# Kernel tuning notes

Measured on AMD Instinct MI355X. Metric: run time of the kernel, lower is better.

The kernel has to match this reference:

```python
import jax, jax.numpy as jnp
import numpy as np


def setup_inputs() -> dict:
    key = jax.random.key(0)
    ks = jax.random.split(key, 9)
    B, D_IN, UNITS, TOPICS, VOCAB = 64, 512, 1024, 20, 32000
    return {
        "inputs": jax.random.normal(ks[0], (B, D_IN), jnp.float32),
        "prev_state": jax.random.normal(ks[1], (B, UNITS), jnp.float32),
        "kernel": jax.random.normal(ks[2], (D_IN, UNITS), jnp.float32) * 0.02,
        "recurrent_kernel": jax.random.normal(ks[3], (UNITS, UNITS), jnp.float32) * 0.02,
        "bernoli_kernel": jax.random.normal(ks[4], (UNITS, 1), jnp.float32) * 0.02,
        "vocab_kernel": jax.random.normal(ks[5], (UNITS, VOCAB), jnp.float32) * 0.02,
        "beta": jax.random.normal(ks[6], (TOPICS, VOCAB), jnp.float32),
        "indicators": jax.random.randint(ks[7], (B,), 0, 2, jnp.int32),
        "indices": jax.random.randint(ks[8], (B,), 0, VOCAB, jnp.int32),
    }


def reference(inputs, prev_state, kernel, recurrent_kernel, bernoli_kernel,
              vocab_kernel, beta, indicators, indices):
    # h_t = x @ W_xh + h_{t-1} @ W_hh   -> [B, units]
    next_state = inputs @ kernel + prev_state @ recurrent_kernel
    # stop-word Bernoulli prob: sigmoid(softplus(h_t @ w_b))  -> [B, 1]
    bern_p = jax.nn.sigmoid(jax.nn.softplus(next_state @ bernoli_kernel))
    bern_p = bern_p[..., None]  # [B, 1, 1]
    # deterministic sampling key (reference baseline)
    samp_key = jax.random.key(42)
    bern_samples = jax.random.bernoulli(samp_key, bern_p).astype(jnp.float32)
    # logits: [B,1,V] + (1 - l_t) * beta[T,V] -> [B, T, V]
    logits = (next_state @ vocab_kernel)[:, None, :] + (1.0 - bern_samples) * beta
    word_prob_out = jax.nn.softmax(logits, axis=-1)
    return word_prob_out, next_state
```

## Files before the change

kernel.cpp:

```cpp
#include <hip/hip_runtime.h>
#include <cstdint>
#include <cstddef>

typedef unsigned int u32;
typedef unsigned short u16;

#define NB 64
#define DIN 512
#define UNITS 1024
#define TOPICS 20
#define VOCAB 32000
#define NS_OFF ((size_t)NB * TOPICS * VOCAB)
#define ESV_PART ((size_t)NB * VOCAB)

typedef __attribute__((ext_vector_type(8))) short s16x8;
typedef __attribute__((ext_vector_type(4))) float f32x4;

__device__ __forceinline__ float bf2f(u16 h) {
    union { u32 u; float f; } c; c.u = ((u32)h) << 16; return c.f;
}
__device__ __forceinline__ u16 f2bf(float f) {
    union { float f; u32 u; } c; c.f = f;
    u32 r = c.u + 0x7FFFu + ((c.u >> 16) & 1u);
    return (u16)(r >> 16);
}
template<bool F32>
__device__ __forceinline__ float ldv(const void* p, size_t i) {
    if constexpr (F32) return ((const float*)p)[i];
    else return bf2f(((const u16*)p)[i]);
}
__device__ __forceinline__ float ldr(const void* p, size_t i, bool f32) {
    return f32 ? ((const float*)p)[i] : bf2f(((const u16*)p)[i]);
}

__device__ __forceinline__ u32 threefry_bits_partitionable(u32 i) {
    const u32 ks0 = 0u, ks1 = 42u, ks2 = 0u ^ 42u ^ 0x1BD11BDAu;
    u32 x0 = 0u + ks0, x1 = i + ks1;
#define TF_R(r) { x0 += x1; x1 = (x1 << r) | (x1 >> (32 - r)); x1 ^= x0; }
    TF_R(13) TF_R(15) TF_R(26) TF_R(6)
    x0 += ks1; x1 += ks2 + 1u;
    TF_R(17) TF_R(29) TF_R(16) TF_R(24)
    x0 += ks2; x1 += ks0 + 2u;
    TF_R(13) TF_R(15) TF_R(26) TF_R(6)
    x0 += ks0; x1 += ks1 + 3u;
    TF_R(17) TF_R(29) TF_R(16) TF_R(24)
    x0 += ks1; x1 += ks2 + 4u;
    TF_R(13) TF_R(15) TF_R(26) TF_R(6)
    x0 += ks2; x1 += ks0 + 5u;
#undef TF_R
    return x0 ^ x1;
}

__global__ __launch_bounds__(256)
void k_init(const void* __restrict__ beta, int* __restrict__ flag,
            float* __restrict__ lsum, float* __restrict__ eb) {
    int tid = threadIdx.x, lane = tid & 63, w = tid >> 6;
    __shared__ int cnt_s[4];
    int cnt = 0;
    const u32* braw = (const u32*)beta;
    for (int i = tid; i < 1024; i += 256) {
        u32 x = braw[i];
        u32 e = (x >> 7) & 0xFFu;
        cnt += (e >= 110u && e <= 132u) ? 1 : 0;
    }
    for (int off = 32; off; off >>= 1) cnt += __shfl_down(cnt, off, 64);
    if (lane == 0) cnt_s[w] = cnt;
    __syncthreads();
    int total = cnt_s[0] + cnt_s[1] + cnt_s[2] + cnt_s[3];
    bool f32 = total < 512;

    size_t base = (size_t)blockIdx.x * 2000;
    for (int i = tid; i < 2000; i += 256)
        eb[base + i] = __expf(ldr(beta, base + i, f32));

    if (blockIdx.x == 0) {
        for (int i = tid; i < NB * TOPICS; i += 256) lsum[i] = 0.f;
        if (tid == 0) flag[0] = f32 ? 1 : 0;
    }
}

template<bool F32>
__device__ void state_body(const void* xin, const void* h0, const void* Wxh,
                           const void* Whh, float* ns_p) {
    __shared__ float lx[768];
    int bid  = blockIdx.x;
    int b    = bid >> 3;
    int uq   = (bid >> 1) & 3;
    int half = bid & 1;
    int u = (uq << 8) | threadIdx.x;
    for (int i = threadIdx.x; i < 768; i += 256) {
        int kk = half * 768 + i;
        lx[i] = (kk < DIN) ? ldv<F32>(xin, (size_t)b * DIN + kk)
                           : ldv<F32>(h0,  (size_t)b * UNITS + (kk - DIN));
    }
    __syncthreads();
    float acc = 0.f;
    if (half == 0) {
#pragma unroll 8
        for (int k = 0; k < DIN; ++k) acc += lx[k] * ldv<F32>(Wxh, (size_t)k * UNITS + u);
#pragma unroll 8
        for (int k = 0; k < 256; ++k) acc += lx[DIN + k] * ldv<F32>(Whh, (size_t)k * UNITS + u);
    } else {
#pragma unroll 8
        for (int k = 0; k < 768; ++k) acc += lx[k] * ldv<F32>(Whh, (size_t)(256 + k) * UNITS + u);
    }
    ns_p[half * (NB * UNITS) + b * UNITS + u] = acc;
}
__global__ __launch_bounds__(256)
void k_state(const int* __restrict__ flag, const void* xin, const void* h0,
             const void* Wxh, const void* Whh, float* __restrict__ ns_p) {
    if (*flag) state_body<true>(xin, h0, Wxh, Whh, ns_p);
    else       state_body<false>(xin, h0, Wxh, Whh, ns_p);
}

template<bool F32>
__device__ void bern_body(const float* ns_p, const void* bk, float* coeff,
                          float* ns_f32, void* dout) {
    int b = blockIdx.x, lane = threadIdx.x;
    float s = 0.f;
#pragma unroll
    for (int i = 0; i < UNITS / 64; ++i) {
        int k = lane + (i << 6);
        int idx = b * UNITS + k;
        float v = ns_p[idx] + ns_p[NB * UNITS + idx];
        ns_f32[idx] = v;
        if constexpr (F32) ((float*)dout)[NS_OFF + idx] = v;
        else               ((u16*)dout)[NS_OFF + idx]   = f2bf(v);
        s += v * ldv<F32>(bk, k);
    }
    for (int off = 32; off; off >>= 1) s += __shfl_down(s, off, 64);
    if (lane == 0) {
        float sp = log1pf(expf(s));
        float p  = 1.f / (1.f + expf(-sp));
        u32 bits = threefry_bits_partitionable((u32)b);
        union { u32 u; float f; } c; c.u = (bits >> 9) | 0x3f800000u;
        float uni = c.f - 1.0f;
        coeff[b] = (uni < p) ? 0.f : 1.f;
    }
}
__global__ __launch_bounds__(64)
void k_bern(const int* __restrict__ flag, const float* __restrict__ ns_p,
            const void* bk, float* __restrict__ coeff,
            float* __restrict__ ns_f32, void* dout) {
    if (*flag) bern_body<true>(ns_p, bk, coeff, ns_f32, dout);
    else       bern_body<false>(ns_p, bk, coeff, ns_f32, dout);
}

#define PAD 68
#define SV_BB 4096
#define SV_SMEM_BYTES 34816

__device__ void sv_mfma_body(const short* __restrict__ ns16,
                             const short* __restrict__ Wv,
                             float* __restrict__ esv4, char* smem,
                             int pos, int kb) {
    const int tid  = threadIdx.x;
    const int lane = tid & 63;
    const int wn   = tid >> 6;
    const int g    = lane >> 4;
    const int l15  = lane & 15;

    const int v0 = pos * 64;
    const int kbase0 = kb * 256;

    const int bk_ = tid >> 3, bc_ = tid & 7;
    const short* bsrc = Wv + (size_t)(kbase0 + bk_) * VOCAB + v0
                      + ((bc_ ^ (bk_ >> 3)) << 3);
    const short* as0 = ns16 + (size_t)(l15     ) * UNITS + kbase0 + g * 8;
    const short* as1 = ns16 + (size_t)(l15 + 16) * UNITS + kbase0 + g * 8;
    const short* as2 = ns16 + (size_t)(l15 + 32) * UNITS + kbase0 + g * 8;
    const short* as3 = ns16 + (size_t)(l15 + 48) * UNITS + kbase0 + g * 8;

    float4 bE, bO;
    s16x8  aE0, aE1, aE2, aE3;
    s16x8  aO0, aO1, aO2, aO3;

    f32x4 acc[4];
#pragma unroll
    for (int m = 0; m < 4; ++m) acc[m] = (f32x4){0.f, 0.f, 0.f, 0.f};

#define LOADB(T, R)  { R = *(const float4*)(bsrc + (size_t)(T) * 32 * VOCAB); }
#define LOADA(T, A0, A1, A2, A3) {                                        \
    int ko = (T) * 32;                                                    \
    A0 = *(const s16x8*)(as0 + ko); A1 = *(const s16x8*)(as1 + ko);       \
    A2 = *(const s16x8*)(as2 + ko); A3 = *(const s16x8*)(as3 + ko); }
#define WRITEB(BUF, R)  { ((float4*)(smem + (BUF) * SV_BB))[tid] = R; }
#define COMPUTE(BUF, A0, A1, A2, A3) {                                    \
    const short* Bs = (const short*)(smem + (BUF) * SV_BB);               \
    int col = wn * 16 + l15;                                              \
    int b0  = (((col >> 3) ^ g) << 3) + (col & 7);                        \
    s16x8 bf;                                                             \
    _Pragma("unroll")                                                     \
    for (int e = 0; e < 8; ++e) bf[e] = Bs[(g * 8 + e) * 64 + b0];        \
    acc[0] = __builtin_amdgcn_mfma_f32_16x16x32_bf16(A0, bf, acc[0], 0, 0, 0); \
    acc[1] = __builtin_amdgcn_mfma_f32_16x16x32_bf16(A1, bf, acc[1], 0, 0, 0); \
    acc[2] = __builtin_amdgcn_mfma_f32_16x16x32_bf16(A2, bf, acc[2], 0, 0, 0); \
    acc[3] = __builtin_amdgcn_mfma_f32_16x16x32_bf16(A3, bf, acc[3], 0, 0, 0); }
#define VMW(N)  asm volatile("s_waitcnt vmcnt(" #N ")" ::: "memory");
#define LGK0    asm volatile("s_waitcnt lgkmcnt(0)" ::: "memory");
#define BAR     __builtin_amdgcn_s_barrier();

    LOADB(0, bE)
    LOADA(0, aE0, aE1, aE2, aE3)
    LOADB(1, bO)
    VMW(5)
    WRITEB(0, bE)
    LGK0

    LOADB(2, bE)  LOADA(1, aO0, aO1, aO2, aO3)
    BAR  VMW(5)  WRITEB(1, bO)  LGK0
    COMPUTE(0, aE0, aE1, aE2, aE3)
    LOADB(3, bO)  LOADA(2, aE0, aE1, aE2, aE3)
    BAR  VMW(5)  WRITEB(0, bE)  LGK0
    COMPUTE(1, aO0, aO1, aO2, aO3)
    LOADB(4, bE)  LOADA(3, aO0, aO1, aO2, aO3)
    BAR  VMW(5)  WRITEB(1, bO)  LGK0
    COMPUTE(2, aE0, aE1, aE2, aE3)
    LOADB(5, bO)  LOADA(4, aE0, aE1, aE2, aE3)
    BAR  VMW(5)  WRITEB(0, bE)  LGK0
    COMPUTE(3, aO0, aO1, aO2, aO3)
    LOADB(6, bE)  LOADA(5, aO0, aO1, aO2, aO3)
    BAR  VMW(5)  WRITEB(1, bO)  LGK0
    COMPUTE(4, aE0, aE1, aE2, aE3)
    LOADB(7, bO)  LOADA(6, aE0, aE1, aE2, aE3)
    BAR  VMW(5)  WRITEB(0, bE)  LGK0
    COMPUTE(5, aO0, aO1, aO2, aO3)
    LOADA(7, aO0, aO1, aO2, aO3)
    BAR  VMW(4)  WRITEB(1, bO)  LGK0
    COMPUTE(6, aE0, aE1, aE2, aE3)
    BAR  VMW(0)
    COMPUTE(7, aO0, aO1, aO2, aO3)

#undef LOADB
#undef LOADA
#undef WRITEB
#undef COMPUTE
#undef VMW
#undef LGK0
#undef BAR

    float* dst = esv4 + (size_t)kb * ESV_PART + v0;
    const int col = wn * 16 + l15;
#pragma unroll
    for (int mf = 0; mf < 4; ++mf)
#pragma unroll
        for (int r = 0; r < 4; ++r) {
            int b = mf * 16 + (lane >> 4) * 4 + r;
            dst[(size_t)b * VOCAB + col] = acc[mf][r];
        }
}

__device__ void sv_f32_body(const float* __restrict__ ns, const float* __restrict__ Wv,
                            float* __restrict__ esv4, float* As, float* Bs,
                            int pos, int kb) {
    int tid = threadIdx.x;
    int vt = tid & 7;
    int bg = tid >> 3;
    int v0 = pos * 64;
    float acc[2][8];
#pragma unroll
    for (int r = 0; r < 2; ++r)
#pragma unroll
        for (int j = 0; j < 8; ++j) acc[r][j] = 0.f;

    for (int k0 = kb * 256; k0 < kb * 256 + 256; k0 += 64) {
        __syncthreads();
        for (int e = tid; e < 1024; e += 256) {
            int row = e >> 4, c4 = e & 15;
            *(float4*)&As[row * PAD + c4 * 4] =
                *(const float4*)&ns[row * UNITS + k0 + c4 * 4];
        }
        for (int e = tid; e < 1024; e += 256) {
            int row = e >> 4, c4 = e & 15;
            *(float4*)&Bs[row * PAD + c4 * 4] =
                *(const float4*)(Wv + (size_t)(k0 + row) * VOCAB + v0 + c4 * 4);
        }
        __syncthreads();
#pragma unroll 4
        for (int u = 0; u < 64; u += 4) {
            float4 a0 = *(float4*)&As[(bg * 2 + 0) * PAD + u];
            float4 a1 = *(float4*)&As[(bg * 2 + 1) * PAD + u];
            float aa0[4] = {a0.x, a0.y, a0.z, a0.w};
            float aa1[4] = {a1.x, a1.y, a1.z, a1.w};
#pragma unroll
            for (int uu = 0; uu < 4; ++uu) {
                float4 b0 = *(float4*)&Bs[(u + uu) * PAD + vt * 8];
                float4 b1 = *(float4*)&Bs[(u + uu) * PAD + vt * 8 + 4];
                float bb[8] = {b0.x, b0.y, b0.z, b0.w, b1.x, b1.y, b1.z, b1.w};
#pragma unroll
                for (int j = 0; j < 8; ++j) {
                    acc[0][j] = fmaf(aa0[uu], bb[j], acc[0][j]);
                    acc[1][j] = fmaf(aa1[uu], bb[j], acc[1][j]);
                }
            }
        }
    }
    float* base = esv4 + (size_t)kb * ESV_PART;
#pragma unroll
    for (int r = 0; r < 2; ++r) {
        float4 e0 = {acc[r][0], acc[r][1], acc[r][2], acc[r][3]};
        float4 e1 = {acc[r][4], acc[r][5], acc[r][6], acc[r][7]};
        float* dst = base + (size_t)(bg * 2 + r) * VOCAB + v0 + vt * 8;
        *(float4*)dst = e0;
        *(float4*)(dst + 4) = e1;
    }
}

__global__ __launch_bounds__(256, 3)
void k_sv(const int* __restrict__ flag, const float* __restrict__ ns,
          const void* Wv, const void* dout, float* __restrict__ esv4, int kb) {
    __shared__ __align__(16) char smem[SV_SMEM_BYTES];
    int lin = blockIdx.x;
    int xcd = lin & 7, idx = lin >> 3;
    int pos = (xcd < 4) ? xcd * 63 + idx : 252 + (xcd - 4) * 62 + idx;
    if (*flag) {
        float* As = (float*)smem;
        sv_f32_body(ns, (const float*)Wv, esv4, As, As + 64 * PAD, pos, kb);
    } else {
        sv_mfma_body((const short*)dout + NS_OFF, (const short*)Wv, esv4, smem,
                     pos, kb);
    }
}

__global__ __launch_bounds__(256)
void k_sum(const float* __restrict__ esv4, const float* __restrict__ eb,
           const float* __restrict__ coeff, float* __restrict__ lsum) {
    int b = blockIdx.y, tid = threadIdx.x;
    float c = coeff[b];
    const float4* P0 = (const float4*)(esv4 + (size_t)b * VOCAB);
    const float4* P1 = (const float4*)(esv4 + ESV_PART + (size_t)b * VOCAB);
    const float4* P2 = (const float4*)(esv4 + 2 * ESV_PART + (size_t)b * VOCAB);
    const float4* P3 = (const float4*)(esv4 + 3 * ESV_PART + (size_t)b * VOCAB);
    int i0 = blockIdx.x * 256 + tid;
    __shared__ float red[4][TOPICS];
    int lane = tid & 63, w = tid >> 6;

    if (c != 0.f) {
        float acc[TOPICS];
#pragma unroll
        for (int t = 0; t < TOPICS; ++t) acc[t] = 0.f;
        for (int i = i0; i < VOCAB / 4; i += 4096) {
            float4 q = P0[i];
            float4 a = P1[i], d = P2[i], h = P3[i];
            q.x += a.x + d.x + h.x; q.y += a.y + d.y + h.y;
            q.z += a.z + d.z + h.z; q.w += a.w + d.w + h.w;
            float4 e;
            e.x = __expf(q.x); e.y = __expf(q.y);
            e.z = __expf(q.z); e.w = __expf(q.w);
#pragma unroll
            for (int t = 0; t < TOPICS; ++t) {
                float4 g = *(const float4*)(eb + (size_t)t * VOCAB + i * 4);
                acc[t] += e.x * g.x + e.y * g.y + e.z * g.z + e.w * g.w;
            }
        }
#pragma unroll
        for (int t = 0; t < TOPICS; ++t) {
            float v = acc[t];
            for (int off = 32; off; off >>= 1) v += __shfl_down(v, off, 64);
            if (lane == 0) red[w][t] = v;
        }
        __syncthreads();
        if (tid < TOPICS) {
            float s = red[0][tid] + red[1][tid] + red[2][tid] + red[3][tid];
            atomicAdd(&lsum[b * TOPICS + tid], s);
        }
    } else {
        float a = 0.f;
        for (int i = i0; i < VOCAB / 4; i += 4096) {
            float4 q = P0[i];
            float4 x = P1[i], d = P2[i], h = P3[i];
            q.x += x.x + d.x + h.x; q.y += x.y + d.y + h.y;
            q.z += x.z + d.z + h.z; q.w += x.w + d.w + h.w;
            a += __expf(q.x) + __expf(q.y) + __expf(q.z) + __expf(q.w);
        }
        for (int off = 32; off; off >>= 1) a += __shfl_down(a, off, 64);
        if (lane == 0) red[w][0] = a;
        __syncthreads();
        if (tid < TOPICS) {
            float s = red[0][0] + red[1][0] + red[2][0] + red[3][0];
            atomicAdd(&lsum[b * TOPICS + tid], s);
        }
    }
}

template<bool F32>
__device__ void write_body(const float* esv4, const float* eb, const float* coeff,
                           const float* lsum, void* dout) {
    int b = blockIdx.y, tid = threadIdx.x;
    int v0 = blockIdx.x * 2048 + tid * 8;
    if (v0 >= VOCAB) return;
    float c = coeff[b];
    const float* er = esv4 + (size_t)b * VOCAB + v0;
    float4 q0 = *(const float4*)er;
    float4 q1 = *(const float4*)(er + 4);
#pragma unroll
    for (int p = 1; p < 4; ++p) {
        float4 a0 = *(const float4*)(er + p * ESV_PART);
        float4 a1 = *(const float4*)(er + p * ESV_PART + 4);
        q0.x += a0.x; q0.y += a0.y; q0.z += a0.z; q0.w += a0.w;
        q1.x += a1.x; q1.y += a1.y; q1.z += a1.z; q1.w += a1.w;
    }
    float4 e0, e1;
    e0.x = __expf(q0.x); e0.y = __expf(q0.y); e0.z = __expf(q0.z); e0.w = __expf(q0.w);
    e1.x = __expf(q1.x); e1.y = __expf(q1.y); e1.z = __expf(q1.z); e1.w = __expf(q1.w);
#pragma unroll 4
    for (int t = 0; t < TOPICS; ++t) {
        float inv = 1.0f / lsum[b * TOPICS + t];
        float o0, o1, o2, o3, o4, o5, o6, o7;
        if (c != 0.f) {
            const float* gr = eb + (size_t)t * VOCAB + v0;
            float4 g0 = *(const float4*)gr;
            float4 g1 = *(const float4*)(gr + 4);
            o0 = e0.x * g0.x * inv; o1 = e0.y * g0.y * inv;
            o2 = e0.z * g0.z * inv; o3 = e0.w * g0.w * inv;
            o4 = e1.x * g1.x * inv; o5 = e1.y * g1.y * inv;
            o6 = e1.z * g1.z * inv; o7 = e1.w * g1.w * inv;
        } else {
            o0 = e0.x * inv; o1 = e0.y * inv; o2 = e0.z * inv; o3 = e0.w * inv;
            o4 = e1.x * inv; o5 = e1.y * inv; o6 = e1.z * inv; o7 = e1.w * inv;
        }
        size_t off = (size_t)b * TOPICS * VOCAB + (size_t)t * VOCAB + v0;
        if constexpr (F32) {
            float4 s0 = {o0, o1, o2, o3}, s1 = {o4, o5, o6, o7};
            *(float4*)((float*)dout + off) = s0;
            *(float4*)((float*)dout + off + 4) = s1;
        } else {
            uint4 st;
            st.x = (u32)f2bf(o0) | ((u32)f2bf(o1) << 16);
            st.y = (u32)f2bf(o2) | ((u32)f2bf(o3) << 16);
            st.z = (u32)f2bf(o4) | ((u32)f2bf(o5) << 16);
            st.w = (u32)f2bf(o6) | ((u32)f2bf(o7) << 16);
            *(uint4*)((u16*)dout + off) = st;
        }
    }
}
__global__ __launch_bounds__(256)
void k_write(const int* __restrict__ flag, const float* __restrict__ esv4,
             const float* __restrict__ eb, const float* __restrict__ coeff,
             const float* __restrict__ lsum, void* dout) {
    if (*flag) write_body<true>(esv4, eb, coeff, lsum, dout);
    else       write_body<false>(esv4, eb, coeff, lsum, dout);
}

extern "C" void kernel_launch(void* const* d_in, const int* in_sizes, int n_in,
                              void* d_out, int out_size, void* d_ws, size_t ws_size,
                              hipStream_t stream) {
    const void* xin  = d_in[0];
    const void* h0   = d_in[1];
    const void* Wxh  = d_in[2];
    const void* Whh  = d_in[3];
    const void* bk   = d_in[4];
    const void* Wv   = d_in[5];
    const void* beta = d_in[6];

    char* ws = (char*)d_ws;
    int*   flag   = (int*)  (ws + 0);
    float* coeff  = (float*)(ws + 256);
    float* lsum   = (float*)(ws + 1024);
    float* ns_f32 = (float*)(ws + 8192);
    float* eb     = (float*)(ws + 270336);
    float* esv4   = (float*)(ws + 2830336);
    float* ns_p   = esv4;

    k_init <<<320, 256, 0, stream>>>(beta, flag, lsum, eb);
    k_state<<<512, 256, 0, stream>>>(flag, xin, h0, Wxh, Whh, ns_p);
    k_bern <<<64, 64, 0, stream>>>(flag, ns_p, bk, coeff, ns_f32, d_out);
    k_sv   <<<500, 256, 0, stream>>>(flag, ns_f32, Wv, d_out, esv4, 0);
    k_sv   <<<500, 256, 0, stream>>>(flag, ns_f32, Wv, d_out, esv4, 1);
    k_sv   <<<500, 256, 0, stream>>>(flag, ns_f32, Wv, d_out, esv4, 2);
    k_sv   <<<500, 256, 0, stream>>>(flag, ns_f32, Wv, d_out, esv4, 3);
    k_sum  <<<dim3(16, 64), 256, 0, stream>>>(esv4, eb, coeff, lsum);
    k_write<<<dim3(16, 64), 256, 0, stream>>>(flag, esv4, eb, coeff, lsum, d_out);
}
```

Before: 464.3 us.

## Fuse init into state kernel, merge split-K launches, cache exp in sum

Folds the init kernel (dtype detection, exp(beta), lsum zeroing) into extra blocks of the state kernel. Each block now detects the dtype locally instead of reading a flag. The four k_sv split-K launches become a single 2000-block launch. k_sum now stores the combined exp(logits) into a new buffer, so k_write reads one array instead of four partials and skips the exp. This cuts launch overhead and the write kernel's memory traffic, at the cost of an extra 8MB write in k_sum and redundant beta sampling in every state block.

Measured after the change: 406.7 us. 12.4% less time.

```diff
diff --git a/kernel.cpp b/kernel.cpp
--- a/kernel.cpp
+++ b/kernel.cpp
@@ -31,6 +31,22 @@
 }
 __device__ __forceinline__ float ldr(const void* p, size_t i, bool f32) {
     return f32 ? ((const float*)p)[i] : bf2f(((const u16*)p)[i]);
+}
+
+__device__ __forceinline__ bool detect_f32(const void* beta) {
+    __shared__ int cnt_s[4];
+    int tid = threadIdx.x, lane = tid & 63, w = tid >> 6;
+    int cnt = 0;
+    const u32* braw = (const u32*)beta;
+    for (int i = tid; i < 1024; i += 256) {
+        u32 e = (braw[i] >> 7) & 0xFFu;
+        cnt += (e >= 110u && e <= 132u) ? 1 : 0;
+    }
+    for (int off = 32; off; off >>= 1) cnt += __shfl_down(cnt, off, 64);
+    if (lane == 0) cnt_s[w] = cnt;
+    __syncthreads();
+    int total = cnt_s[0] + cnt_s[1] + cnt_s[2] + cnt_s[3];
+    return total < 512;
 }
 
 __device__ __forceinline__ u32 threefry_bits_partitionable(u32 i) {
@@ -51,34 +67,6 @@
     return x0 ^ x1;
 }
 
-__global__ __launch_bounds__(256)
-void k_init(const void* __restrict__ beta, int* __restrict__ flag,
-            float* __restrict__ lsum, float* __restrict__ eb) {
-    int tid = threadIdx.x, lane = tid & 63, w = tid >> 6;
-    __shared__ int cnt_s[4];
-    int cnt = 0;
-    const u32* braw = (const u32*)beta;
-    for (int i = tid; i < 1024; i += 256) {
-        u32 x = braw[i];
-        u32 e = (x >> 7) & 0xFFu;
-        cnt += (e >= 110u && e <= 132u) ? 1 : 0;
-    }
-    for (int off = 32; off; off >>= 1) cnt += __shfl_down(cnt, off, 64);
-    if (lane == 0) cnt_s[w] = cnt;
-    __syncthreads();
-    int total = cnt_s[0] + cnt_s[1] + cnt_s[2] + cnt_s[3];
-    bool f32 = total < 512;
-
-    size_t base = (size_t)blockIdx.x * 2000;
-    for (int i = tid; i < 2000; i += 256)
-        eb[base + i] = __expf(ldr(beta, base + i, f32));
-
-    if (blockIdx.x == 0) {
-        for (int i = tid; i < NB * TOPICS; i += 256) lsum[i] = 0.f;
-        if (tid == 0) flag[0] = f32 ? 1 : 0;
-    }
-}
-
 template<bool F32>
 __device__ void state_body(const void* xin, const void* h0, const void* Wxh,
                            const void* Whh, float* ns_p) {
@@ -107,10 +95,24 @@
     ns_p[half * (NB * UNITS) + b * UNITS + u] = acc;
 }
 __global__ __launch_bounds__(256)
-void k_state(const int* __restrict__ flag, const void* xin, const void* h0,
-             const void* Wxh, const void* Whh, float* __restrict__ ns_p) {
-    if (*flag) state_body<true>(xin, h0, Wxh, Whh, ns_p);
-    else       state_body<false>(xin, h0, Wxh, Whh, ns_p);
+void k_state(const void* __restrict__ beta, const void* xin, const void* h0,
+             const void* Wxh, const void* Whh, float* __restrict__ ns_p,
+             int* __restrict__ flag, float* __restrict__ lsum,
+             float* __restrict__ eb) {
+    bool f32 = detect_f32(beta);
+    int bid = blockIdx.x, tid = threadIdx.x;
+    if (bid >= 512) {
+        size_t base = (size_t)(bid - 512) * 2000;
+        for (int i = tid; i < 2000; i += 256)
+            eb[base + i] = __expf(ldr(beta, base + i, f32));
+        if (bid == 512) {
+            for (int i = tid; i < NB * TOPICS; i += 256) lsum[i] = 0.f;
+            if (tid == 0) flag[0] = f32 ? 1 : 0;
+        }
+        return;
+    }
+    if (f32) state_body<true>(xin, h0, Wxh, Whh, ns_p);
+    else     state_body<false>(xin, h0, Wxh, Whh, ns_p);
 }
 
 template<bool F32>
@@ -308,10 +310,12 @@
 
 __global__ __launch_bounds__(256, 3)
 void k_sv(const int* __restrict__ flag, const float* __restrict__ ns,
-          const void* Wv, const void* dout, float* __restrict__ esv4, int kb) {
+          const void* Wv, const void* dout, float* __restrict__ esv4) {
     __shared__ __align__(16) char smem[SV_SMEM_BYTES];
     int lin = blockIdx.x;
-    int xcd = lin & 7, idx = lin >> 3;
+    int kb  = lin / 500;
+    int q   = lin - kb * 500;
+    int xcd = q & 7, idx = q >> 3;
     int pos = (xcd < 4) ? xcd * 63 + idx : 252 + (xcd - 4) * 62 + idx;
     if (*flag) {
         float* As = (float*)smem;
@@ -324,13 +328,15 @@
 
 __global__ __launch_bounds__(256)
 void k_sum(const float* __restrict__ esv4, const float* __restrict__ eb,
-           const float* __restrict__ coeff, float* __restrict__ lsum) {
+           const float* __restrict__ coeff, float* __restrict__ lsum,
+           float* __restrict__ esv_c) {
     int b = blockIdx.y, tid = threadIdx.x;
     float c = coeff[b];
     const float4* P0 = (const float4*)(esv4 + (size_t)b * VOCAB);
     const float4* P1 = (const float4*)(esv4 + ESV_PART + (size_t)b * VOCAB);
     const float4* P2 = (const float4*)(esv4 + 2 * ESV_PART + (size_t)b * VOCAB);
     const float4* P3 = (const float4*)(esv4 + 3 * ESV_PART + (size_t)b * VOCAB);
+    float4* EC = (float4*)(esv_c + (size_t)b * VOCAB);
     int i0 = blockIdx.x * 256 + tid;
     __shared__ float red[4][TOPICS];
     int lane = tid & 63, w = tid >> 6;
@@ -347,6 +353,7 @@
             float4 e;
             e.x = __expf(q.x); e.y = __expf(q.y);
             e.z = __expf(q.z); e.w = __expf(q.w);
+            EC[i] = e;
 #pragma unroll
             for (int t = 0; t < TOPICS; ++t) {
                 float4 g = *(const float4*)(eb + (size_t)t * VOCAB + i * 4);
@@ -371,7 +378,11 @@
             float4 x = P1[i], d = P2[i], h = P3[i];
             q.x += x.x + d.x + h.x; q.y += x.y + d.y + h.y;
             q.z += x.z + d.z + h.z; q.w += x.w + d.w + h.w;
-            a += __expf(q.x) + __expf(q.y) + __expf(q.z) + __expf(q.w);
+            float4 e;
+            e.x = __expf(q.x); e.y = __expf(q.y);
+            e.z = __expf(q.z); e.w = __expf(q.w);
+            EC[i] = e;
+            a += e.x + e.y + e.z + e.w;
         }
         for (int off = 32; off; off >>= 1) a += __shfl_down(a, off, 64);
         if (lane == 0) red[w][0] = a;
@@ -384,25 +395,15 @@
 }
 
 template<bool F32>
-__device__ void write_body(const float* esv4, const float* eb, const float* coeff,
+__device__ void write_body(const float* esv_c, const float* eb, const float* coeff,
                            const float* lsum, void* dout) {
     int b = blockIdx.y, tid = threadIdx.x;
     int v0 = blockIdx.x * 2048 + tid * 8;
     if (v0 >= VOCAB) return;
     float c = coeff[b];
-    const float* er = esv4 + (size_t)b * VOCAB + v0;
-    float4 q0 = *(const float4*)er;
-    float4 q1 = *(const float4*)(er + 4);
-#pragma unroll
-    for (int p = 1; p < 4; ++p) {
-        float4 a0 = *(const float4*)(er + p * ESV_PART);
-        float4 a1 = *(const float4*)(er + p * ESV_PART + 4);
-        q0.x += a0.x; q0.y += a0.y; q0.z += a0.z; q0.w += a0.w;
-        q1.x += a1.x; q1.y += a1.y; q1.z += a1.z; q1.w += a1.w;
-    }
-    float4 e0, e1;
-    e0.x = __expf(q0.x); e0.y = __expf(q0.y); e0.z = __expf(q0.z); e0.w = __expf(q0.w);
-    e1.x = __expf(q1.x); e1.y = __expf(q1.y); e1.z = __expf(q1.z); e1.w = __expf(q1.w);
+    const float* er = esv_c + (size_t)b * VOCAB + v0;
+    float4 e0 = *(const float4*)er;
+    float4 e1 = *(const float4*)(er + 4);
 #pragma unroll 4
     for (int t = 0; t < TOPICS; ++t) {
         float inv = 1.0f / lsum[b * TOPICS + t];
@@ -435,11 +436,11 @@
     }
 }
 __global__ __launch_bounds__(256)
-void k_write(const int* __restrict__ flag, const float* __restrict__ esv4,
+void k_write(const int* __restrict__ flag, const float* __restrict__ esv_c,
              const float* __restrict__ eb, const float* __restrict__ coeff,
              const float* __restrict__ lsum, void* dout) {
-    if (*flag) write_body<true>(esv4, eb, coeff, lsum, dout);
-    else       write_body<false>(esv4, eb, coeff, lsum, dout);
+    if (*flag) write_body<true>(esv_c, eb, coeff, lsum, dout);
+    else       write_body<false>(esv_c, eb, coeff, lsum, dout);
 }
 
 extern "C" void kernel_launch(void* const* d_in, const int* in_sizes, int n_in,
@@ -460,15 +461,12 @@
     float* ns_f32 = (float*)(ws + 8192);
     float* eb     = (float*)(ws + 270336);
     float* esv4   = (float*)(ws + 2830336);
+    float* esv_c  = (float*)(ws + 35598336);
     float* ns_p   = esv4;
 
-    k_init <<<320, 256, 0, stream>>>(beta, flag, lsum, eb);
-    k_state<<<512, 256, 0, stream>>>(flag, xin, h0, Wxh, Whh, ns_p);
+    k_state<<<832, 256, 0, stream>>>(beta, xin, h0, Wxh, Whh, ns_p, flag, lsum, eb);
     k_bern <<<64, 64, 0, stream>>>(flag, ns_p, bk, coeff, ns_f32, d_out);
-    k_sv   <<<500, 256, 0, stream>>>(flag, ns_f32, Wv, d_out, esv4, 0);
-    k_sv   <<<500, 256, 0, stream>>>(flag, ns_f32, Wv, d_out, esv4, 1);
-    k_sv   <<<500, 256, 0, stream>>>(flag, ns_f32, Wv, d_out, esv4, 2);
-    k_sv   <<<500, 256, 0, stream>>>(flag, ns_f32, Wv, d_out, esv4, 3);
-    k_sum  <<<dim3(16, 64), 256, 0, stream>>>(esv4, eb, coeff, lsum);
-    k_write<<<dim3(16, 64), 256, 0, stream>>>(flag, esv4, eb, coeff, lsum, d_out);
-}
+    k_sv   <<<2000, 256, 0, stream>>>(flag, ns_f32, Wv, d_out, esv4);
+    k_sum  <<<dim3(16, 64), 256, 0, stream>>>(esv4, eb, coeff, lsum, esv_c);
+    k_write<<<dim3(16, 64), 256, 0, stream>>>(flag, esv_c, eb, coeff, lsum, d_out);
+}
```
